# Optimization experiments

Measured on AMD Instinct MI355X. Metric: run time of the kernel, lower is better.

Reference implementation:

```python
import jax, jax.numpy as jnp
import numpy as np

B, T, D = 4, 2048, 2048
H = 16
Q_RANK, KV_RANK = 1536, 512
NOPE, ROPE_D, V_D = 128, 64, 128
QK_D = NOPE + ROPE_D  # 192
D_FF = 8192
EPS = 1e-6
THETA = 10000.0
SCALE = QK_D ** -0.5  # mscale = 1 (no rope_scaling)


def _w(key, shape):
    fan_in = shape[0]
    return jax.random.normal(key, shape, dtype=jnp.float32) / np.sqrt(fan_in)


def setup_inputs() -> dict:
    key = jax.random.key(0)
    ks = jax.random.split(key, 16)
    return {
        "x": jax.random.normal(ks[0], (B, T, D), dtype=jnp.float32),
        "ln1_w": jnp.ones((D,), jnp.float32),
        "wq_a": _w(ks[1], (D, Q_RANK)),
        "q_a_ln_w": jnp.ones((Q_RANK,), jnp.float32),
        "wq_b": _w(ks[2], (Q_RANK, H * QK_D)),
        "wkv_a": _w(ks[3], (D, KV_RANK + ROPE_D)),
        "kv_a_ln_w": jnp.ones((KV_RANK,), jnp.float32),
        "wkv_b": _w(ks[4], (KV_RANK, H * (NOPE + V_D))),
        "wo": _w(ks[5], (H * V_D, D)),
        "ln2_w": jnp.ones((D,), jnp.float32),
        "w_gate": _w(ks[6], (D, D_FF)),
        "w_up": _w(ks[7], (D, D_FF)),
        "w_down": _w(ks[8], (D_FF, D)),
        "attention_mask": jnp.ones((B, T), jnp.int32),
        "positions": jnp.broadcast_to(jnp.arange(T, dtype=jnp.int32), (B, T)),
    }


def rmsnorm(x, w):
    return x * jax.lax.rsqrt(jnp.mean(x * x, axis=-1, keepdims=True) + EPS) * w


def apply_rope(x, positions):
    # x: [B, T, h, d], positions: [B, T]
    d = x.shape[-1]
    inv_freq = 1.0 / (THETA ** (jnp.arange(0, d, 2, dtype=jnp.float32) / d))
    ang = positions.astype(jnp.float32)[:, :, None] * inv_freq  # [B,T,d/2]
    cos = jnp.cos(ang)[:, :, None, :]
    sin = jnp.sin(ang)[:, :, None, :]
    x1, x2 = jnp.split(x, 2, axis=-1)
    return jnp.concatenate([x1 * cos - x2 * sin, x2 * cos + x1 * sin], axis=-1)


def reference(x, ln1_w, wq_a, q_a_ln_w, wq_b, wkv_a, kv_a_ln_w, wkv_b, wo,
              ln2_w, w_gate, w_up, w_down, attention_mask, positions):
    # --- MLA attention block ---
    h = rmsnorm(x, ln1_w)
    # low-rank q projection
    q = rmsnorm(h @ wq_a, q_a_ln_w) @ wq_b            # [B,T,H*192]
    q = q.reshape(B, T, H, QK_D)
    q_pass, q_rot = jnp.split(q, [NOPE], axis=-1)
    # compressed kv + shared rope key
    ckv = h @ wkv_a                                    # [B,T,512+64]
    k_c, k_rot = jnp.split(ckv, [KV_RANK], axis=-1)
    k_rot = k_rot.reshape(B, T, 1, ROPE_D)
    kv = rmsnorm(k_c, kv_a_ln_w) @ wkv_b               # [B,T,H*(128+128)]
    kv = kv.reshape(B, T, H, NOPE + V_D)
    k_pass, v = jnp.split(kv, [NOPE], axis=-1)
    # split RoPE on rope dims only
    q_rot = apply_rope(q_rot, positions)
    k_rot = jnp.broadcast_to(apply_rope(k_rot, positions), (B, T, H, ROPE_D))
    qh = jnp.concatenate([q_pass, q_rot], axis=-1)     # [B,T,H,192]
    kh = jnp.concatenate([k_pass, k_rot], axis=-1)     # [B,T,H,192]
    # attention with causal + padding mask (V pad-to-192 then slice is a no-op mathematically)
    scores = jnp.einsum('bqhd,bkhd->bhqk', qh, kh) * SCALE
    causal = jnp.tril(jnp.ones((T, T), bool))
    mask = causal[None, None] & attention_mask[:, None, None, :].astype(bool)
    scores = jnp.where(mask, scores, jnp.finfo(scores.dtype).min)
    attn = jax.nn.softmax(scores, axis=-1)
    o = jnp.einsum('bhqk,bkhd->bqhd', attn, v).reshape(B, T, H * V_D)
    x = x + o @ wo
    # --- MLP block ---
    h2 = rmsnorm(x, ln2_w)
    mlp = (jax.nn.silu(h2 @ w_gate) * (h2 @ w_up)) @ w_down
    return x + mlp
```

## Files before the change

kernel.cpp:

```cpp
#include <hip/hip_runtime.h>

typedef float f32x4 __attribute__((ext_vector_type(4)));
typedef __bf16 bf16x8 __attribute__((ext_vector_type(8)));
typedef unsigned short u16x8 __attribute__((ext_vector_type(8)));
typedef unsigned short u16x4 __attribute__((ext_vector_type(4)));

static __device__ __forceinline__ unsigned short f2b(float f) {
  union { float f; unsigned u; } v; v.f = f;
  unsigned r = v.u + 0x7fffu + ((v.u >> 16) & 1u);
  return (unsigned short)(r >> 16);
}
static __device__ __forceinline__ float b2f(unsigned short s) {
  union { unsigned u; float f; } v; v.u = ((unsigned)s) << 16;
  return v.f;
}
static __device__ __forceinline__ void gload_lds16(const unsigned short* g, unsigned short* l) {
  __builtin_amdgcn_global_load_lds((const __attribute__((address_space(1))) void*)g,
                                   (__attribute__((address_space(3))) void*)l, 16, 0, 0);
}

#define NEG_BIG -3.0e38f

__global__ __launch_bounds__(256) void fill_sentinel(float* __restrict__ out, int n, float v) {
  int i = blockIdx.x * 256 + threadIdx.x;
  if (i < n) out[i] = v;
}

__global__ __launch_bounds__(256) void transpose_convert(const float* __restrict__ in,
                                                         unsigned short* __restrict__ out,
                                                         int K, int N, int in_ld, int row0, int col0) {
  __shared__ float tile[32][33];
  const int k0 = blockIdx.y * 32, n0 = blockIdx.x * 32;
  const int tx = threadIdx.x & 31, ty = threadIdx.x >> 5;
#pragma unroll
  for (int i = 0; i < 32; i += 8) {
    int k = k0 + ty + i, n = n0 + tx;
    tile[ty + i][tx] = (k < K && n < N) ? in[(size_t)(row0 + k) * in_ld + col0 + n] : 0.f;
  }
  __syncthreads();
#pragma unroll
  for (int i = 0; i < 32; i += 8) {
    int n = n0 + ty + i, k = k0 + tx;
    if (n < N && k < K) out[(size_t)n * K + k] = f2b(tile[tx][ty + i]);
  }
}

__global__ __launch_bounds__(256) void rmsnorm_kernel(const float* __restrict__ in,
                                                      const float* __restrict__ w,
                                                      unsigned short* __restrict__ out,
                                                      int ncols, int in_stride, int out_stride) {
  const int row = blockIdx.x;
  const float* rp = in + (size_t)row * in_stride;
  const int n4 = ncols >> 2;
  float4 v[2];
  int nv = 0;
  float ss = 0.f;
  for (int c = threadIdx.x; c < n4; c += 256) {
    float4 xv = reinterpret_cast<const float4*>(rp)[c];
    v[nv++] = xv;
    ss += xv.x * xv.x + xv.y * xv.y + xv.z * xv.z + xv.w * xv.w;
  }
#pragma unroll
  for (int m = 32; m; m >>= 1) ss += __shfl_xor(ss, m);
  __shared__ float red[4];
  if ((threadIdx.x & 63) == 0) red[threadIdx.x >> 6] = ss;
  __syncthreads();
  const float total = red[0] + red[1] + red[2] + red[3];
  const float scale = rsqrtf(total / (float)ncols + 1e-6f);
  nv = 0;
  unsigned short* op = out + (size_t)row * out_stride;
  for (int c = threadIdx.x; c < n4; c += 256) {
    float4 xv = v[nv++];
    float4 wv = reinterpret_cast<const float4*>(w)[c];
    u16x4 o;
    o[0] = f2b(xv.x * scale * wv.x);
    o[1] = f2b(xv.y * scale * wv.y);
    o[2] = f2b(xv.z * scale * wv.z);
    o[3] = f2b(xv.w * scale * wv.w);
    reinterpret_cast<u16x4*>(op)[c] = o;
  }
}

template <int EPI>
__global__ __launch_bounds__(256) void gemm_bt(const unsigned short* __restrict__ A,
                                               const unsigned short* __restrict__ Bt,
                                               float* __restrict__ outf,
                                               unsigned short* __restrict__ outb,
                                               const float* __restrict__ res,
                                               const unsigned short* __restrict__ aux,
                                               int M, int N, int K) {
  __shared__ __align__(16) unsigned short As[128 * 32];
  __shared__ __align__(16) unsigned short Bs[128 * 32];
  const int tid = threadIdx.x;
  const int l = tid & 63;
  const int lr = l & 15, lg = l >> 4;
  const int wr = tid >> 7, wc = (tid >> 6) & 1;

  const int gx = gridDim.x;
  const int nwg = gx * gridDim.y;
  int lin = blockIdx.y * gx + blockIdx.x;
  {
    const int qq = nwg >> 3, rr = nwg & 7;
    const int xcd = lin & 7, idx = lin >> 3;
    lin = (xcd < rr ? xcd * (qq + 1) : rr * (qq + 1) + (xcd - rr) * qq) + idx;
  }
  const int m0 = (lin / gx) * 128, n0 = (lin % gx) * 128;

  f32x4 acc[4][4] = {};

  for (int k0 = 0; k0 < K; k0 += 32) {
#pragma unroll
    for (int j = 0; j < 2; ++j) {
      const int chunk = j * 256 + tid;
      const int row = chunk >> 2, kc = chunk & 3;
      const unsigned short* ga = A + (size_t)(m0 + row) * K + k0 + kc * 8;
      gload_lds16(ga, &As[(size_t)(j * 256 + (tid & 192)) * 8]);
      int rb = n0 + row;
      if (rb > N - 1) rb = N - 1;
      const unsigned short* gb = Bt + (size_t)rb * K + k0 + kc * 8;
      gload_lds16(gb, &Bs[(size_t)(j * 256 + (tid & 192)) * 8]);
    }
    __syncthreads();
    bf16x8 af[4], bfr[4];
#pragma unroll
    for (int mi = 0; mi < 4; ++mi)
      af[mi] = *reinterpret_cast<const bf16x8*>(&As[(wr * 64 + mi * 16 + lr) * 32 + lg * 8]);
#pragma unroll
    for (int ni = 0; ni < 4; ++ni)
      bfr[ni] = *reinterpret_cast<const bf16x8*>(&Bs[(wc * 64 + ni * 16 + lr) * 32 + lg * 8]);
#pragma unroll
    for (int mi = 0; mi < 4; ++mi)
#pragma unroll
      for (int ni = 0; ni < 4; ++ni)
        acc[mi][ni] = __builtin_amdgcn_mfma_f32_16x16x32_bf16(af[mi], bfr[ni], acc[mi][ni], 0, 0, 0);
    __syncthreads();
  }

#pragma unroll
  for (int mi = 0; mi < 4; ++mi) {
#pragma unroll
    for (int ni = 0; ni < 4; ++ni) {
      const int r0 = m0 + wr * 64 + mi * 16 + lg * 4;
      const int c = n0 + wc * 64 + ni * 16 + lr;
      if (c < N) {
#pragma unroll
        for (int j = 0; j < 4; ++j) {
          const size_t idx = (size_t)(r0 + j) * N + c;
          const float v = acc[mi][ni][j];
          if constexpr (EPI == 0) outf[idx] = v;
          else if constexpr (EPI == 1) outb[idx] = f2b(v);
          else if constexpr (EPI == 2) outf[idx] = v + res[idx];
          else if constexpr (EPI == 3) outb[idx] = f2b(v / (1.f + __expf(-v)));
          else outb[idx] = f2b(v * b2f(aux[idx]));
        }
      }
    }
  }
}

template <int EPI>
__global__ __launch_bounds__(512, 1) void gemm256(const unsigned short* __restrict__ A,
                                                  const unsigned short* __restrict__ Bt,
                                                  float* __restrict__ outf,
                                                  unsigned short* __restrict__ outb,
                                                  const float* __restrict__ res,
                                                  const unsigned short* __restrict__ aux,
                                                  int M, int N, int K) {
  __shared__ __align__(16) unsigned short Lds[2][2][2][8192];
  const int tid = threadIdx.x;
  const int l = tid & 63, lr = l & 15, lg = l >> 4;
  const int w = tid >> 6, wr = w >> 2, wn = w & 3;

  const int gn = N >> 8;
  int lin = blockIdx.x;
  {
    const int nwg = gridDim.x;
    lin = (lin & 7) * (nwg >> 3) + (lin >> 3);
  }
  const int m0 = (lin / gn) * 256, n0 = (lin % gn) * 256;

  const int NT = K >> 6;
  const int swz = (lg ^ ((lr >> 1) & 3)) * 8;

  f32x4 acc[8][4] = {};

  auto stageh = [&](int mat, int kh, int t) {
    const unsigned short* src = mat ? Bt : A;
    const int rb = mat ? n0 : m0;
    const int d = t & 1;
#pragma unroll
    for (int g = 0; g < 2; ++g) {
      const int c = g * 512 + tid;
      const int row = c >> 2;
      const int kc = (c & 3) ^ ((row >> 1) & 3);
      gload_lds16(src + (size_t)(rb + row) * K + t * 64 + kh * 32 + kc * 8,
                  &Lds[d][mat][kh][(size_t)(g * 512 + (tid & ~63)) * 8]);
    }
  };

  stageh(0, 0, 0); stageh(1, 0, 0); stageh(0, 1, 0); stageh(1, 1, 0);
  asm volatile("s_waitcnt vmcnt(4)" ::: "memory");
  __builtin_amdgcn_s_barrier();
  __builtin_amdgcn_sched_barrier(0);

  for (int t = 0; t < NT; ++t) {
    const int d = t & 1;
    const bool pf = (t + 1 < NT);
    bf16x8 af[4], bfv[4];

#define RD_A(mh, kk, i)                                                                    \
  af[i] = *reinterpret_cast<const bf16x8*>(                                                \
      &Lds[d][0][kk][(wr * 128 + ((mh) * 4 + (i)) * 16 + lr) * 32 + swz])
#define RD_B(kk, ni)                                                                       \
  bfv[ni] = *reinterpret_cast<const bf16x8*>(                                              \
      &Lds[d][1][kk][(wn * 64 + (ni) * 16 + lr) * 32 + swz])
#define MFMA16(mh)                                                                         \
  _Pragma("unroll") for (int i = 0; i < 4; ++i)                                            \
  _Pragma("unroll") for (int ni = 0; ni < 4; ++ni)                                         \
      acc[(mh) * 4 + i][ni] =                                                              \
          __builtin_amdgcn_mfma_f32_16x16x32_bf16(af[i], bfv[ni], acc[(mh) * 4 + i][ni], 0, 0, 0)

    RD_A(0, 0, 0); RD_A(0, 0, 1); RD_A(0, 0, 2); RD_A(0, 0, 3);
    RD_B(0, 0); RD_B(0, 1); RD_B(0, 2); RD_B(0, 3);
    if (pf) stageh(0, 0, t + 1);
    __builtin_amdgcn_s_barrier();
    asm volatile("s_waitcnt lgkmcnt(0)" ::: "memory");
    __builtin_amdgcn_sched_barrier(0);
    __builtin_amdgcn_s_setprio(1);
    MFMA16(0);
    __builtin_amdgcn_s_setprio(0);
    __builtin_amdgcn_s_barrier();

    RD_A(1, 0, 0); RD_A(1, 0, 1); RD_A(1, 0, 2); RD_A(1, 0, 3);
    if (pf) stageh(1, 0, t + 1);
    __builtin_amdgcn_s_barrier();
    asm volatile("s_waitcnt lgkmcnt(0)" ::: "memory");
    __builtin_amdgcn_sched_barrier(0);
    __builtin_amdgcn_s_setprio(1);
    MFMA16(1);
    __builtin_amdgcn_s_setprio(0);
    __builtin_amdgcn_sched_barrier(0);
    if (pf) asm volatile("s_waitcnt vmcnt(4)" ::: "memory");
    else    asm volatile("s_waitcnt vmcnt(0)" ::: "memory");
    __builtin_amdgcn_s_barrier();
    __builtin_amdgcn_sched_barrier(0);

    RD_A(0, 1, 0); RD_A(0, 1, 1); RD_A(0, 1, 2); RD_A(0, 1, 3);
    RD_B(1, 0); RD_B(1, 1); RD_B(1, 2); RD_B(1, 3);
    if (pf) stageh(0, 1, t + 1);
    __builtin_amdgcn_s_barrier();
    asm volatile("s_waitcnt lgkmcnt(0)" ::: "memory");
    __builtin_amdgcn_sched_barrier(0);
    __builtin_amdgcn_s_setprio(1);
    MFMA16(0);
    __builtin_amdgcn_s_setprio(0);
    __builtin_amdgcn_s_barrier();

    RD_A(1, 1, 0); RD_A(1, 1, 1); RD_A(1, 1, 2); RD_A(1, 1, 3);
    if (pf) stageh(1, 1, t + 1);
    __builtin_amdgcn_s_barrier();
    asm volatile("s_waitcnt lgkmcnt(0)" ::: "memory");
    __builtin_amdgcn_sched_barrier(0);
    __builtin_amdgcn_s_setprio(1);
    MFMA16(1);
    __builtin_amdgcn_s_setprio(0);
    __builtin_amdgcn_sched_barrier(0);
    if (pf) asm volatile("s_waitcnt vmcnt(4)" ::: "memory");
    __builtin_amdgcn_s_barrier();
    __builtin_amdgcn_sched_barrier(0);

#undef RD_A
#undef RD_B
#undef MFMA16
  }

#pragma unroll
  for (int mi = 0; mi < 8; ++mi) {
#pragma unroll
    for (int ni = 0; ni < 4; ++ni) {
      const int r = m0 + wr * 128 + mi * 16 + lg * 4;
      const int c = n0 + wn * 64 + ni * 16 + lr;
#pragma unroll
      for (int j = 0; j < 4; ++j) {
        const size_t idx = (size_t)(r + j) * N + c;
        const float v = acc[mi][ni][j];
        if constexpr (EPI == 0) outf[idx] = v;
        else if constexpr (EPI == 1) outb[idx] = f2b(v);
        else if constexpr (EPI == 2) outf[idx] = v + res[idx];
        else if constexpr (EPI == 3) outb[idx] = f2b(v / (1.f + __expf(-v)));
        else outb[idx] = f2b(v * b2f(aux[idx]));
      }
    }
  }
}

__global__ __launch_bounds__(256) void rope_scale_q(unsigned short* __restrict__ q,
                                                    const int* __restrict__ positions) {
  const int row = blockIdx.x;
  const int pos = positions[row];
  unsigned short* qp = q + (size_t)row * 3072;
  const int tid = threadIdx.x;
  const float SCALE = 0.07216878364870322f;
#pragma unroll
  for (int i = 0; i < 8; ++i) {
    int e = i * 256 + tid;
    int hh = e >> 7, d = e & 127;
    int idx = hh * 192 + d;
    qp[idx] = f2b(b2f(qp[idx]) * SCALE);
  }
#pragma unroll
  for (int i = 0; i < 2; ++i) {
    int e = i * 256 + tid;
    int hh = e >> 5, j = e & 31;
    int base = hh * 192 + 128;
    float x1 = b2f(qp[base + j]), x2 = b2f(qp[base + 32 + j]);
    float freq = __expf(-(float)j * (9.210340371976184f / 32.f));
    float sa, ca;
    __sincosf((float)pos * freq, &sa, &ca);
    qp[base + j] = f2b((x1 * ca - x2 * sa) * SCALE);
    qp[base + 32 + j] = f2b((x2 * ca + x1 * sa) * SCALE);
  }
}

__global__ __launch_bounds__(256) void repack_k(const unsigned short* __restrict__ kv,
                                                const float* __restrict__ ckv,
                                                const int* __restrict__ positions,
                                                unsigned short* __restrict__ kh) {
  const int row = blockIdx.x;
  const int tid = threadIdx.x;
  {
    const int hh = tid >> 4, db = tid & 15;
    u16x8 v = *reinterpret_cast<const u16x8*>(kv + (size_t)row * 4096 + hh * 256 + db * 8);
    *reinterpret_cast<u16x8*>(kh + (size_t)row * 3072 + hh * 192 + db * 8) = v;
  }
  __shared__ float o1[32], o2[32];
  if (tid < 32) {
    const int j = tid;
    float x1 = ckv[(size_t)row * 576 + 512 + j];
    float x2 = ckv[(size_t)row * 576 + 544 + j];
    const int pos = positions[row];
    float freq = __expf(-(float)j * (9.210340371976184f / 32.f));
    float sa, ca;
    __sincosf((float)pos * freq, &sa, &ca);
    o1[j] = x1 * ca - x2 * sa;
    o2[j] = x2 * ca + x1 * sa;
  }
  __syncthreads();
#pragma unroll
  for (int i = 0; i < 4; ++i) {
    int e = i * 256 + tid;
    int hh = e >> 6, d = e & 63;
    float v = (d < 32) ? o1[d] : o2[d - 32];
    kh[(size_t)row * 3072 + hh * 192 + 128 + d] = f2b(v);
  }
}

__global__ __launch_bounds__(512) void mla_attn(const unsigned short* __restrict__ qh,
                                                const unsigned short* __restrict__ kh,
                                                const unsigned short* __restrict__ kv,
                                                unsigned short* __restrict__ o) {
  const int T = 2048, H = 16;
  const int qt = (int)gridDim.x - 1 - (int)blockIdx.x;
  const int b = blockIdx.y >> 4;
  const int h = blockIdx.y & 15;
  const int tid = threadIdx.x, w = tid >> 6, l = tid & 63;
  const int lg = l >> 4, lr = l & 15;

  __shared__ __align__(16) unsigned short Ks[64 * 200];
  __shared__ __align__(16) unsigned short Vts[128 * 64];
  __shared__ __align__(16) unsigned short Pl[8][16 * 72];
  __shared__ float exs[8][16];

  int krow[3], kcol[3];
#pragma unroll
  for (int i = 0; i < 3; ++i) { int c = i * 512 + tid; krow[i] = c / 24; kcol[i] = (c % 24) * 8; }
  const int vkvp = tid >> 4;
  const int vf0 = (tid & 15) * 8;

  const unsigned short* kbase0 = kh + (((size_t)b * T) * H + h) * 192;
  const unsigned short* vbase0 = kv + (((size_t)b * T) * H + h) * 256 + 128;

  bf16x8 qa[6];
  {
    const size_t qrow = (size_t)b * T + qt * 128 + w * 16 + lr;
    const unsigned short* qp = qh + (qrow * H + h) * 192 + lg * 8;
#pragma unroll
    for (int kc = 0; kc < 6; ++kc)
      qa[kc] = *reinterpret_cast<const bf16x8*>(qp + kc * 32);
  }

  u16x8 kreg[3], vregA, vregB;
#pragma unroll
  for (int i = 0; i < 3; ++i)
    kreg[i] = *reinterpret_cast<const u16x8*>(kbase0 + (size_t)krow[i] * 3072 + kcol[i]);
  vregA = *reinterpret_cast<const u16x8*>(vbase0 + (size_t)(2 * vkvp) * 4096 + vf0);
  vregB = *reinterpret_cast<const u16x8*>(vbase0 + (size_t)(2 * vkvp + 1) * 4096 + vf0);

  f32x4 ot[8] = {};
  f32x4 lacc = {};
  float mrow[4] = {NEG_BIG, NEG_BIG, NEG_BIG, NEG_BIG};
  bf16x8 ones;
#pragma unroll
  for (int e = 0; e < 8; ++e) ones[e] = (__bf16)1.0f;

  const int ktmax = 2 * qt + 1;
  for (int kt = 0; kt <= ktmax; ++kt) {
#pragma unroll
    for (int i = 0; i < 3; ++i)
      *reinterpret_cast<u16x8*>(&Ks[krow[i] * 200 + kcol[i]]) = kreg[i];
    {
      const int c7 = (vf0 >> 3) & 7;
#pragma unroll
      for (int e = 0; e < 8; ++e) {
        const int blk = (vkvp >> 2) ^ (e ^ c7);
        const unsigned val = (unsigned)(unsigned short)vregA[e] |
                             ((unsigned)(unsigned short)vregB[e] << 16);
        *reinterpret_cast<unsigned*>(&Vts[(vf0 + e) * 64 + blk * 8 + (vkvp & 3) * 2]) = val;
      }
    }
    __syncthreads();

    if (kt < ktmax) {
      const unsigned short* kb = kbase0 + (size_t)(kt + 1) * 64 * 3072;
      const unsigned short* vb = vbase0 + (size_t)(kt + 1) * 64 * 4096;
#pragma unroll
      for (int i = 0; i < 3; ++i)
        kreg[i] = *reinterpret_cast<const u16x8*>(kb + (size_t)krow[i] * 3072 + kcol[i]);
      vregA = *reinterpret_cast<const u16x8*>(vb + (size_t)(2 * vkvp) * 4096 + vf0);
      vregB = *reinterpret_cast<const u16x8*>(vb + (size_t)(2 * vkvp + 1) * 4096 + vf0);
    }

    f32x4 s4[4];
#pragma unroll
    for (int ni = 0; ni < 4; ++ni) {
      f32x4 a = {};
#pragma unroll
      for (int kc = 0; kc < 6; ++kc) {
        bf16x8 kf = *reinterpret_cast<const bf16x8*>(&Ks[(ni * 16 + lr) * 200 + kc * 32 + lg * 8]);
        a = __builtin_amdgcn_mfma_f32_16x16x32_bf16(qa[kc], kf, a, 0, 0, 0);
      }
      s4[ni] = a;
    }
    if (kt >= 2 * qt) {
#pragma unroll
      for (int ni = 0; ni < 4; ++ni) {
        const int colr = ni * 16 + lr;
#pragma unroll
        for (int j = 0; j < 4; ++j) {
          const int qrl = qt * 128 + w * 16 + lg * 4 + j - kt * 64;
          if (colr > qrl) s4[ni][j] = NEG_BIG;
        }
      }
    }

    float pmj[4];
    int need = 0;
#pragma unroll
    for (int j = 0; j < 4; ++j) {
      pmj[j] = fmaxf(fmaxf(s4[0][j], s4[1][j]), fmaxf(s4[2][j], s4[3][j]));
      need |= (pmj[j] > mrow[j] + 8.f) ? 1 : 0;
    }
    if (__any(need)) {
      float al[4];
#pragma unroll
      for (int j = 0; j < 4; ++j) {
        float rm = pmj[j];
#pragma unroll
        for (int m = 1; m < 16; m <<= 1) rm = fmaxf(rm, __shfl_xor(rm, m));
        const float mn = fmaxf(mrow[j], rm);
        al[j] = __expf(mrow[j] - mn);
        mrow[j] = mn;
      }
      if (lr == 0) {
#pragma unroll
        for (int j = 0; j < 4; ++j) exs[w][lg * 4 + j] = al[j];
      }
      const float af = exs[w][lr];
#pragma unroll
      for (int mi = 0; mi < 8; ++mi) {
        ot[mi][0] *= af; ot[mi][1] *= af; ot[mi][2] *= af; ot[mi][3] *= af;
      }
      lacc[0] *= af; lacc[1] *= af; lacc[2] *= af; lacc[3] *= af;
    }

#pragma unroll
    for (int ni = 0; ni < 4; ++ni)
#pragma unroll
      for (int j = 0; j < 4; ++j)
        Pl[w][(lg * 4 + j) * 72 + ni * 16 + lr] = f2b(__expf(s4[ni][j] - mrow[j]));

    bf16x8 pf0 = *reinterpret_cast<const bf16x8*>(&Pl[w][lr * 72 + lg * 8]);
    bf16x8 pf1 = *reinterpret_cast<const bf16x8*>(&Pl[w][lr * 72 + 32 + lg * 8]);
    lacc = __builtin_amdgcn_mfma_f32_16x16x32_bf16(ones, pf0, lacc, 0, 0, 0);
    lacc = __builtin_amdgcn_mfma_f32_16x16x32_bf16(ones, pf1, lacc, 0, 0, 0);
#pragma unroll
    for (int mi = 0; mi < 8; ++mi) {
      const int f = mi * 16 + lr;
      const int sfz = (f & 7) ^ ((f >> 3) & 7);
      const int blk0 = lg ^ sfz;
      const int blk1 = (4 + lg) ^ sfz;
      bf16x8 vf0r = *reinterpret_cast<const bf16x8*>(&Vts[f * 64 + blk0 * 8]);
      ot[mi] = __builtin_amdgcn_mfma_f32_16x16x32_bf16(vf0r, pf0, ot[mi], 0, 0, 0);
      bf16x8 vf1r = *reinterpret_cast<const bf16x8*>(&Vts[f * 64 + blk1 * 8]);
      ot[mi] = __builtin_amdgcn_mfma_f32_16x16x32_bf16(vf1r, pf1, ot[mi], 0, 0, 0);
    }
    __syncthreads();
  }

  const float li = 1.f / lacc[0];
  const size_t orow = (size_t)b * T + qt * 128 + w * 16 + lr;
#pragma unroll
  for (int mi = 0; mi < 8; ++mi)
#pragma unroll
    for (int j = 0; j < 4; ++j) {
      const int feat = mi * 16 + lg * 4 + j;
      o[orow * 2048 + h * 128 + feat] = f2b(ot[mi][j] * li);
    }
}

extern "C" void kernel_launch(void* const* d_in, const int* in_sizes, int n_in,
                              void* d_out, int out_size, void* d_ws, size_t ws_size,
                              hipStream_t stream) {
  (void)in_sizes; (void)n_in;
  const float* x      = (const float*)d_in[0];
  const float* ln1_w  = (const float*)d_in[1];
  const float* wq_a   = (const float*)d_in[2];
  const float* qaln_w = (const float*)d_in[3];
  const float* wq_b   = (const float*)d_in[4];
  const float* wkv_a  = (const float*)d_in[5];
  const float* kvln_w = (const float*)d_in[6];
  const float* wkv_b  = (const float*)d_in[7];
  const float* wo     = (const float*)d_in[8];
  const float* ln2_w  = (const float*)d_in[9];
  const float* w_gate = (const float*)d_in[10];
  const float* w_up   = (const float*)d_in[11];
  const float* w_down = (const float*)d_in[12];
  const int*   pos    = (const int*)d_in[14];
  float* out = (float*)d_out;

  const int Mt = 8192;

  char* ws = (char*)d_ws;
  const size_t R1 = 0;
  const size_t R2 = R1 + 67108864;
  const size_t R3 = R2 + 50331648;
  const size_t R4 = R3 + 50331648;
  const size_t R5 = R4 + 33554432;
  const size_t R6 = R5 + 18874368;
  const size_t REQ = R6 + 9437184;

  if (ws_size < REQ) {
    fill_sentinel<<<dim3((out_size + 255) / 256), dim3(256), 0, stream>>>(
        out, out_size, (float)(ws_size >> 20));
    return;
  }

  float*          qa_f  = (float*)(ws + R1);
  unsigned short* kvbuf = (unsigned short*)(ws + R1);
  unsigned short* qbuf  = (unsigned short*)(ws + R2);
  unsigned short* qan   = (unsigned short*)(ws + R3);
  unsigned short* ckvn  = (unsigned short*)(ws + R3);
  unsigned short* khbuf = (unsigned short*)(ws + R3);
  unsigned short* hbuf  = (unsigned short*)(ws + R4);
  unsigned short* obuf  = (unsigned short*)(ws + R4);
  float*          ckv   = (float*)(ws + R5);
  unsigned short* slotW = (unsigned short*)(ws + R6);
  unsigned short* actb  = (unsigned short*)(ws + 0);
  unsigned short* h2b   = (unsigned short*)(ws + 134217728);
  unsigned short* wsl2  = (unsigned short*)(ws + 167772160);

  dim3 blk(256);
  dim3 blk5(512);
  auto tcf = [&](const float* W, int K, int N) {
    transpose_convert<<<dim3((N + 31) / 32, (K + 31) / 32), blk, 0, stream>>>(W, slotW, K, N, N, 0, 0);
  };
  auto g256 = [&](auto epi, const unsigned short* Aa, const unsigned short* Bb, float* of,
                  unsigned short* ob, const float* rs, const unsigned short* ax, int N, int K) {
    gemm256<decltype(epi)::value><<<dim3(32 * (N >> 8)), blk5, 0, stream>>>(Aa, Bb, of, ob, rs, ax, Mt, N, K);
  };

  rmsnorm_kernel<<<Mt, blk, 0, stream>>>(x, ln1_w, hbuf, 2048, 2048, 2048);
  tcf(wq_a, 2048, 1536);
  g256(std::integral_constant<int,0>{}, hbuf, slotW, qa_f, nullptr, nullptr, nullptr, 1536, 2048);
  rmsnorm_kernel<<<Mt, blk, 0, stream>>>(qa_f, qaln_w, qan, 1536, 1536, 1536);
  tcf(wq_b, 1536, 3072);
  g256(std::integral_constant<int,1>{}, qan, slotW, nullptr, qbuf, nullptr, nullptr, 3072, 1536);
  tcf(wkv_a, 2048, 576);
  gemm_bt<0><<<dim3(5, 64), blk, 0, stream>>>(hbuf, slotW, ckv, nullptr, nullptr, nullptr, Mt, 576, 2048);
  rmsnorm_kernel<<<Mt, blk, 0, stream>>>(ckv, kvln_w, ckvn, 512, 576, 512);
  tcf(wkv_b, 512, 4096);
  g256(std::integral_constant<int,1>{}, ckvn, slotW, nullptr, kvbuf, nullptr, nullptr, 4096, 512);
  rope_scale_q<<<Mt, blk, 0, stream>>>(qbuf, pos);
  repack_k<<<Mt, blk, 0, stream>>>(kvbuf, ckv, pos, khbuf);
  mla_attn<<<dim3(16, 64), blk5, 0, stream>>>(qbuf, khbuf, kvbuf, obuf);
  tcf(wo, 2048, 2048);
  g256(std::integral_constant<int,2>{}, obuf, slotW, out, nullptr, x, nullptr, 2048, 2048);
  rmsnorm_kernel<<<Mt, blk, 0, stream>>>(out, ln2_w, h2b, 2048, 2048, 2048);
  transpose_convert<<<dim3(256, 64), blk, 0, stream>>>(w_gate, wsl2, 2048, 8192, 8192, 0, 0);
  g256(std::integral_constant<int,3>{}, h2b, wsl2, nullptr, actb, nullptr, nullptr, 8192, 2048);
  transpose_convert<<<dim3(256, 64), blk, 0, stream>>>(w_up, wsl2, 2048, 8192, 8192, 0, 0);
  g256(std::integral_constant<int,4>{}, h2b, wsl2, nullptr, actb, nullptr, actb, 8192, 2048);
  transpose_convert<<<dim3(64, 256), blk, 0, stream>>>(w_down, wsl2, 8192, 2048, 2048, 0, 0);
  g256(std::integral_constant<int,2>{}, actb, wsl2, out, nullptr, out, nullptr, 2048, 8192);
}
```

Baseline: 1.698 ms.

## Deepen GEMM LDS pipeline to four K=32 stages with prefetch distance three

Restructures the 256x256 GEMM main loop from two double-buffered K=64 tiles (each split into two halves) into a four-slot ring of K=32 tiles, prefetching three tiles ahead. The vmcnt waits are adjusted so the tile about to be consumed is ready while two more remain in flight. The aim is to hide global-load latency better without increasing LDS usage. The cost is twice as many loop iterations with their barriers and waits per unit of K.

```diff
diff --git a/kernel.cpp b/kernel.cpp
--- a/kernel.cpp
+++ b/kernel.cpp
@@ -166,7 +166,7 @@
                                                   const float* __restrict__ res,
                                                   const unsigned short* __restrict__ aux,
                                                   int M, int N, int K) {
-  __shared__ __align__(16) unsigned short Lds[2][2][2][8192];
+  __shared__ __align__(16) unsigned short Lds[4][2][8192];
   const int tid = threadIdx.x;
   const int l = tid & 63, lr = l & 15, lg = l >> 4;
   const int w = tid >> 6, wr = w >> 2, wn = w & 3;
@@ -179,50 +179,52 @@
   }
   const int m0 = (lin / gn) * 256, n0 = (lin % gn) * 256;
 
-  const int NT = K >> 6;
+  const int NT = K >> 5;
   const int swz = (lg ^ ((lr >> 1) & 3)) * 8;
 
   f32x4 acc[8][4] = {};
 
-  auto stageh = [&](int mat, int kh, int t) {
+  auto stage_mat = [&](int mat, int t) {
     const unsigned short* src = mat ? Bt : A;
     const int rb = mat ? n0 : m0;
-    const int d = t & 1;
+    const int d = t & 3;
 #pragma unroll
     for (int g = 0; g < 2; ++g) {
       const int c = g * 512 + tid;
       const int row = c >> 2;
       const int kc = (c & 3) ^ ((row >> 1) & 3);
-      gload_lds16(src + (size_t)(rb + row) * K + t * 64 + kh * 32 + kc * 8,
-                  &Lds[d][mat][kh][(size_t)(g * 512 + (tid & ~63)) * 8]);
+      gload_lds16(src + (size_t)(rb + row) * K + t * 32 + kc * 8,
+                  &Lds[d][mat][(size_t)(g * 512 + (tid & ~63)) * 8]);
     }
   };
 
-  stageh(0, 0, 0); stageh(1, 0, 0); stageh(0, 1, 0); stageh(1, 1, 0);
-  asm volatile("s_waitcnt vmcnt(4)" ::: "memory");
+  stage_mat(0, 0); stage_mat(1, 0);
+  stage_mat(0, 1); stage_mat(1, 1);
+  stage_mat(0, 2); stage_mat(1, 2);
+  asm volatile("s_waitcnt vmcnt(8)" ::: "memory");
   __builtin_amdgcn_s_barrier();
   __builtin_amdgcn_sched_barrier(0);
 
   for (int t = 0; t < NT; ++t) {
-    const int d = t & 1;
-    const bool pf = (t + 1 < NT);
+    const int d = t & 3;
+    const bool pf = (t + 3 < NT);
     bf16x8 af[4], bfv[4];
 
-#define RD_A(mh, kk, i)                                                                    \
+#define RD_A(mh, i)                                                                        \
   af[i] = *reinterpret_cast<const bf16x8*>(                                                \
-      &Lds[d][0][kk][(wr * 128 + ((mh) * 4 + (i)) * 16 + lr) * 32 + swz])
-#define RD_B(kk, ni)                                                                       \
+      &Lds[d][0][(wr * 128 + ((mh) * 4 + (i)) * 16 + lr) * 32 + swz])
+#define RD_B(ni)                                                                           \
   bfv[ni] = *reinterpret_cast<const bf16x8*>(                                              \
-      &Lds[d][1][kk][(wn * 64 + (ni) * 16 + lr) * 32 + swz])
+      &Lds[d][1][(wn * 64 + (ni) * 16 + lr) * 32 + swz])
 #define MFMA16(mh)                                                                         \
   _Pragma("unroll") for (int i = 0; i < 4; ++i)                                            \
   _Pragma("unroll") for (int ni = 0; ni < 4; ++ni)                                         \
       acc[(mh) * 4 + i][ni] =                                                              \
           __builtin_amdgcn_mfma_f32_16x16x32_bf16(af[i], bfv[ni], acc[(mh) * 4 + i][ni], 0, 0, 0)
 
-    RD_A(0, 0, 0); RD_A(0, 0, 1); RD_A(0, 0, 2); RD_A(0, 0, 3);
-    RD_B(0, 0); RD_B(0, 1); RD_B(0, 2); RD_B(0, 3);
-    if (pf) stageh(0, 0, t + 1);
+    RD_A(0, 0); RD_A(0, 1); RD_A(0, 2); RD_A(0, 3);
+    RD_B(0); RD_B(1); RD_B(2); RD_B(3);
+    if (pf) stage_mat(0, t + 3);
     __builtin_amdgcn_s_barrier();
     asm volatile("s_waitcnt lgkmcnt(0)" ::: "memory");
     __builtin_amdgcn_sched_barrier(0);
@@ -231,8 +233,8 @@
     __builtin_amdgcn_s_setprio(0);
     __builtin_amdgcn_s_barrier();
 
-    RD_A(1, 0, 0); RD_A(1, 0, 1); RD_A(1, 0, 2); RD_A(1, 0, 3);
-    if (pf) stageh(1, 0, t + 1);
+    RD_A(1, 0); RD_A(1, 1); RD_A(1, 2); RD_A(1, 3);
+    if (pf) stage_mat(1, t + 3);
     __builtin_amdgcn_s_barrier();
     asm volatile("s_waitcnt lgkmcnt(0)" ::: "memory");
     __builtin_amdgcn_sched_barrier(0);
@@ -240,32 +242,12 @@
     MFMA16(1);
     __builtin_amdgcn_s_setprio(0);
     __builtin_amdgcn_sched_barrier(0);
-    if (pf) asm volatile("s_waitcnt vmcnt(4)" ::: "memory");
-    else    asm volatile("s_waitcnt vmcnt(0)" ::: "memory");
-    __builtin_amdgcn_s_barrier();
-    __builtin_amdgcn_sched_barrier(0);
-
-    RD_A(0, 1, 0); RD_A(0, 1, 1); RD_A(0, 1, 2); RD_A(0, 1, 3);
-    RD_B(1, 0); RD_B(1, 1); RD_B(1, 2); RD_B(1, 3);
-    if (pf) stageh(0, 1, t + 1);
-    __builtin_amdgcn_s_barrier();
-    asm volatile("s_waitcnt lgkmcnt(0)" ::: "memory");
-    __builtin_amdgcn_sched_barrier(0);
-    __builtin_amdgcn_s_setprio(1);
-    MFMA16(0);
-    __builtin_amdgcn_s_setprio(0);
-    __builtin_amdgcn_s_barrier();
-
-    RD_A(1, 1, 0); RD_A(1, 1, 1); RD_A(1, 1, 2); RD_A(1, 1, 3);
-    if (pf) stageh(1, 1, t + 1);
-    __builtin_amdgcn_s_barrier();
-    asm volatile("s_waitcnt lgkmcnt(0)" ::: "memory");
-    __builtin_amdgcn_sched_barrier(0);
-    __builtin_amdgcn_s_setprio(1);
-    MFMA16(1);
-    __builtin_amdgcn_s_setprio(0);
-    __builtin_amdgcn_sched_barrier(0);
-    if (pf) asm volatile("s_waitcnt vmcnt(4)" ::: "memory");
+    {
+      const int rem = NT - 1 - t;
+      if (rem >= 3)      asm volatile("s_waitcnt vmcnt(8)" ::: "memory");
+      else if (rem == 2) asm volatile("s_waitcnt vmcnt(4)" ::: "memory");
+      else if (rem == 1) asm volatile("s_waitcnt vmcnt(0)" ::: "memory");
+    }
     __builtin_amdgcn_s_barrier();
     __builtin_amdgcn_sched_barrier(0);
 
```

Result: slower. 1.738 ms (+2.4%).

## Balance causal attention by pairing query tiles, fold q scale into weights, regroup GEMM tiles

Applied to the files above, without the earlier changes.

Each attention workgroup now processes two query tiles, bx and 15-bx, so every block does the same amount of causal work and the grid is halved. The softmax scale is folded into the wq_b weight conversion, which removes the separate scaling pass over the q nope dimensions. The GEMM block index mapping is changed to group eight M-tiles per N column for better L2 reuse. Risks: half as many attention blocks for occupancy, and the q scale is applied before bf16 rounding of the weights, which changes rounding slightly.

```diff
diff --git a/kernel.cpp b/kernel.cpp
--- a/kernel.cpp
+++ b/kernel.cpp
@@ -28,7 +28,8 @@
 
 __global__ __launch_bounds__(256) void transpose_convert(const float* __restrict__ in,
                                                          unsigned short* __restrict__ out,
-                                                         int K, int N, int in_ld, int row0, int col0) {
+                                                         int K, int N, int in_ld, int row0, int col0,
+                                                         float scale) {
   __shared__ float tile[32][33];
   const int k0 = blockIdx.y * 32, n0 = blockIdx.x * 32;
   const int tx = threadIdx.x & 31, ty = threadIdx.x >> 5;
@@ -41,7 +42,7 @@
 #pragma unroll
   for (int i = 0; i < 32; i += 8) {
     int n = n0 + ty + i, k = k0 + tx;
-    if (n < N && k < K) out[(size_t)n * K + k] = f2b(tile[tx][ty + i]);
+    if (n < N && k < K) out[(size_t)n * K + k] = f2b(tile[tx][ty + i] * scale);
   }
 }
 
@@ -177,7 +178,11 @@
     const int nwg = gridDim.x;
     lin = (lin & 7) * (nwg >> 3) + (lin >> 3);
   }
-  const int m0 = (lin / gn) * 256, n0 = (lin % gn) * 256;
+  const int npg = gn << 3;
+  const int gid = lin / npg;
+  const int idx = lin - gid * npg;
+  const int m0 = (gid * 8 + (idx & 7)) * 256;
+  const int n0 = (idx >> 3) * 256;
 
   const int NT = K >> 6;
   const int swz = (lg ^ ((lr >> 1) & 3)) * 8;
@@ -282,32 +287,24 @@
       const int c = n0 + wn * 64 + ni * 16 + lr;
 #pragma unroll
       for (int j = 0; j < 4; ++j) {
-        const size_t idx = (size_t)(r + j) * N + c;
+        const size_t idx2 = (size_t)(r + j) * N + c;
         const float v = acc[mi][ni][j];
-        if constexpr (EPI == 0) outf[idx] = v;
-        else if constexpr (EPI == 1) outb[idx] = f2b(v);
-        else if constexpr (EPI == 2) outf[idx] = v + res[idx];
-        else if constexpr (EPI == 3) outb[idx] = f2b(v / (1.f + __expf(-v)));
-        else outb[idx] = f2b(v * b2f(aux[idx]));
+        if constexpr (EPI == 0) outf[idx2] = v;
+        else if constexpr (EPI == 1) outb[idx2] = f2b(v);
+        else if constexpr (EPI == 2) outf[idx2] = v + res[idx2];
+        else if constexpr (EPI == 3) outb[idx2] = f2b(v / (1.f + __expf(-v)));
+        else outb[idx2] = f2b(v * b2f(aux[idx2]));
       }
     }
   }
 }
 
-__global__ __launch_bounds__(256) void rope_scale_q(unsigned short* __restrict__ q,
-                                                    const int* __restrict__ positions) {
+__global__ __launch_bounds__(256) void rope_q(unsigned short* __restrict__ q,
+                                              const int* __restrict__ positions) {
   const int row = blockIdx.x;
   const int pos = positions[row];
   unsigned short* qp = q + (size_t)row * 3072;
   const int tid = threadIdx.x;
-  const float SCALE = 0.07216878364870322f;
-#pragma unroll
-  for (int i = 0; i < 8; ++i) {
-    int e = i * 256 + tid;
-    int hh = e >> 7, d = e & 127;
-    int idx = hh * 192 + d;
-    qp[idx] = f2b(b2f(qp[idx]) * SCALE);
-  }
 #pragma unroll
   for (int i = 0; i < 2; ++i) {
     int e = i * 256 + tid;
@@ -317,8 +314,8 @@
     float freq = __expf(-(float)j * (9.210340371976184f / 32.f));
     float sa, ca;
     __sincosf((float)pos * freq, &sa, &ca);
-    qp[base + j] = f2b((x1 * ca - x2 * sa) * SCALE);
-    qp[base + 32 + j] = f2b((x2 * ca + x1 * sa) * SCALE);
+    qp[base + j] = f2b(x1 * ca - x2 * sa);
+    qp[base + 32 + j] = f2b(x2 * ca + x1 * sa);
   }
 }
 
@@ -360,7 +357,7 @@
                                                 const unsigned short* __restrict__ kv,
                                                 unsigned short* __restrict__ o) {
   const int T = 2048, H = 16;
-  const int qt = (int)gridDim.x - 1 - (int)blockIdx.x;
+  const int bx = blockIdx.x;
   const int b = blockIdx.y >> 4;
   const int h = blockIdx.y & 15;
   const int tid = threadIdx.x, w = tid >> 6, l = tid & 63;
@@ -380,142 +377,147 @@
   const unsigned short* kbase0 = kh + (((size_t)b * T) * H + h) * 192;
   const unsigned short* vbase0 = kv + (((size_t)b * T) * H + h) * 256 + 128;
 
-  bf16x8 qa[6];
-  {
-    const size_t qrow = (size_t)b * T + qt * 128 + w * 16 + lr;
-    const unsigned short* qp = qh + (qrow * H + h) * 192 + lg * 8;
-#pragma unroll
-    for (int kc = 0; kc < 6; ++kc)
-      qa[kc] = *reinterpret_cast<const bf16x8*>(qp + kc * 32);
-  }
-
-  u16x8 kreg[3], vregA, vregB;
-#pragma unroll
-  for (int i = 0; i < 3; ++i)
-    kreg[i] = *reinterpret_cast<const u16x8*>(kbase0 + (size_t)krow[i] * 3072 + kcol[i]);
-  vregA = *reinterpret_cast<const u16x8*>(vbase0 + (size_t)(2 * vkvp) * 4096 + vf0);
-  vregB = *reinterpret_cast<const u16x8*>(vbase0 + (size_t)(2 * vkvp + 1) * 4096 + vf0);
-
-  f32x4 ot[8] = {};
-  f32x4 lacc = {};
-  float mrow[4] = {NEG_BIG, NEG_BIG, NEG_BIG, NEG_BIG};
   bf16x8 ones;
 #pragma unroll
   for (int e = 0; e < 8; ++e) ones[e] = (__bf16)1.0f;
 
-  const int ktmax = 2 * qt + 1;
-  for (int kt = 0; kt <= ktmax; ++kt) {
+  for (int half = 0; half < 2; ++half) {
+    const int qt = half ? (15 - bx) : bx;
+
+    bf16x8 qa[6];
+    {
+      const size_t qrow = (size_t)b * T + qt * 128 + w * 16 + lr;
+      const unsigned short* qp = qh + (qrow * H + h) * 192 + lg * 8;
+#pragma unroll
+      for (int kc = 0; kc < 6; ++kc)
+        qa[kc] = *reinterpret_cast<const bf16x8*>(qp + kc * 32);
+    }
+
+    u16x8 kreg[3], vregA, vregB;
 #pragma unroll
     for (int i = 0; i < 3; ++i)
-      *reinterpret_cast<u16x8*>(&Ks[krow[i] * 200 + kcol[i]]) = kreg[i];
-    {
-      const int c7 = (vf0 >> 3) & 7;
-#pragma unroll
-      for (int e = 0; e < 8; ++e) {
-        const int blk = (vkvp >> 2) ^ (e ^ c7);
-        const unsigned val = (unsigned)(unsigned short)vregA[e] |
-                             ((unsigned)(unsigned short)vregB[e] << 16);
-        *reinterpret_cast<unsigned*>(&Vts[(vf0 + e) * 64 + blk * 8 + (vkvp & 3) * 2]) = val;
-      }
+      kreg[i] = *reinterpret_cast<const u16x8*>(kbase0 + (size_t)krow[i] * 3072 + kcol[i]);
+    vregA = *reinterpret_cast<const u16x8*>(vbase0 + (size_t)(2 * vkvp) * 4096 + vf0);
+    vregB = *reinterpret_cast<const u16x8*>(vbase0 + (size_t)(2 * vkvp + 1) * 4096 + vf0);
+
+    f32x4 ot[8] = {};
+    f32x4 lacc = {};
+    float mrow[4] = {NEG_BIG, NEG_BIG, NEG_BIG, NEG_BIG};
+
+    const int ktmax = 2 * qt + 1;
+    for (int kt = 0; kt <= ktmax; ++kt) {
+#pragma unroll
+      for (int i = 0; i < 3; ++i)
+        *reinterpret_cast<u16x8*>(&Ks[krow[i] * 200 + kcol[i]]) = kreg[i];
+      {
+        const int c7 = (vf0 >> 3) & 7;
+#pragma unroll
+        for (int e = 0; e < 8; ++e) {
+          const int blk = (vkvp >> 2) ^ (e ^ c7);
+          const unsigned val = (unsigned)(unsigned short)vregA[e] |
+                               ((unsigned)(unsigned short)vregB[e] << 16);
+          *reinterpret_cast<unsigned*>(&Vts[(vf0 + e) * 64 + blk * 8 + (vkvp & 3) * 2]) = val;
+        }
+      }
+      __syncthreads();
+
+      if (kt < ktmax) {
+        const unsigned short* kb = kbase0 + (size_t)(kt + 1) * 64 * 3072;
+        const unsigned short* vb = vbase0 + (size_t)(kt + 1) * 64 * 4096;
+#pragma unroll
+        for (int i = 0; i < 3; ++i)
+          kreg[i] = *reinterpret_cast<const u16x8*>(kb + (size_t)krow[i] * 3072 + kcol[i]);
+        vregA = *reinterpret_cast<const u16x8*>(vb + (size_t)(2 * vkvp) * 4096 + vf0);
+        vregB = *reinterpret_cast<const u16x8*>(vb + (size_t)(2 * vkvp + 1) * 4096 + vf0);
+      }
+
+      f32x4 s4[4];
+#pragma unroll
+      for (int ni = 0; ni < 4; ++ni) {
+        f32x4 a = {};
+#pragma unroll
+        for (int kc = 0; kc < 6; ++kc) {
+          bf16x8 kf = *reinterpret_cast<const bf16x8*>(&Ks[(ni * 16 + lr) * 200 + kc * 32 + lg * 8]);
+          a = __builtin_amdgcn_mfma_f32_16x16x32_bf16(qa[kc], kf, a, 0, 0, 0);
+        }
+        s4[ni] = a;
+      }
+      if (kt >= 2 * qt) {
+#pragma unroll
+        for (int ni = 0; ni < 4; ++ni) {
+          const int colr = ni * 16 + lr;
+#pragma unroll
+          for (int j = 0; j < 4; ++j) {
+            const int qrl = qt * 128 + w * 16 + lg * 4 + j - kt * 64;
+            if (colr > qrl) s4[ni][j] = NEG_BIG;
+          }
+        }
+      }
+
+      float pmj[4];
+      int need = 0;
+#pragma unroll
+      for (int j = 0; j < 4; ++j) {
+        pmj[j] = fmaxf(fmaxf(s4[0][j], s4[1][j]), fmaxf(s4[2][j], s4[3][j]));
+        need |= (pmj[j] > mrow[j] + 8.f) ? 1 : 0;
+      }
+      if (__any(need)) {
+        float al[4];
+#pragma unroll
+        for (int j = 0; j < 4; ++j) {
+          float rm = pmj[j];
+#pragma unroll
+          for (int m = 1; m < 16; m <<= 1) rm = fmaxf(rm, __shfl_xor(rm, m));
+          const float mn = fmaxf(mrow[j], rm);
+          al[j] = __expf(mrow[j] - mn);
+          mrow[j] = mn;
+        }
+        if (lr == 0) {
+#pragma unroll
+          for (int j = 0; j < 4; ++j) exs[w][lg * 4 + j] = al[j];
+        }
+        const float af = exs[w][lr];
+#pragma unroll
+        for (int mi = 0; mi < 8; ++mi) {
+          ot[mi][0] *= af; ot[mi][1] *= af; ot[mi][2] *= af; ot[mi][3] *= af;
+        }
+        lacc[0] *= af; lacc[1] *= af; lacc[2] *= af; lacc[3] *= af;
+      }
+
+#pragma unroll
+      for (int ni = 0; ni < 4; ++ni)
+#pragma unroll
+        for (int j = 0; j < 4; ++j)
+          Pl[w][(lg * 4 + j) * 72 + ni * 16 + lr] = f2b(__expf(s4[ni][j] - mrow[j]));
+
+      bf16x8 pf0 = *reinterpret_cast<const bf16x8*>(&Pl[w][lr * 72 + lg * 8]);
+      bf16x8 pf1 = *reinterpret_cast<const bf16x8*>(&Pl[w][lr * 72 + 32 + lg * 8]);
+      lacc = __builtin_amdgcn_mfma_f32_16x16x32_bf16(ones, pf0, lacc, 0, 0, 0);
+      lacc = __builtin_amdgcn_mfma_f32_16x16x32_bf16(ones, pf1, lacc, 0, 0, 0);
+#pragma unroll
+      for (int mi = 0; mi < 8; ++mi) {
+        const int f = mi * 16 + lr;
+        const int sfz = (f & 7) ^ ((f >> 3) & 7);
+        const int blk0 = lg ^ sfz;
+        const int blk1 = (4 + lg) ^ sfz;
+        bf16x8 vf0r = *reinterpret_cast<const bf16x8*>(&Vts[f * 64 + blk0 * 8]);
+        ot[mi] = __builtin_amdgcn_mfma_f32_16x16x32_bf16(vf0r, pf0, ot[mi], 0, 0, 0);
+        bf16x8 vf1r = *reinterpret_cast<const bf16x8*>(&Vts[f * 64 + blk1 * 8]);
+        ot[mi] = __builtin_amdgcn_mfma_f32_16x16x32_bf16(vf1r, pf1, ot[mi], 0, 0, 0);
+      }
+      __syncthreads();
     }
-    __syncthreads();
-
-    if (kt < ktmax) {
-      const unsigned short* kb = kbase0 + (size_t)(kt + 1) * 64 * 3072;
-      const unsigned short* vb = vbase0 + (size_t)(kt + 1) * 64 * 4096;
-#pragma unroll
-      for (int i = 0; i < 3; ++i)
-        kreg[i] = *reinterpret_cast<const u16x8*>(kb + (size_t)krow[i] * 3072 + kcol[i]);
-      vregA = *reinterpret_cast<const u16x8*>(vb + (size_t)(2 * vkvp) * 4096 + vf0);
-      vregB = *reinterpret_cast<const u16x8*>(vb + (size_t)(2 * vkvp + 1) * 4096 + vf0);
-    }
-
-    f32x4 s4[4];
-#pragma unroll
-    for (int ni = 0; ni < 4; ++ni) {
-      f32x4 a = {};
-#pragma unroll
-      for (int kc = 0; kc < 6; ++kc) {
-        bf16x8 kf = *reinterpret_cast<const bf16x8*>(&Ks[(ni * 16 + lr) * 200 + kc * 32 + lg * 8]);
-        a = __builtin_amdgcn_mfma_f32_16x16x32_bf16(qa[kc], kf, a, 0, 0, 0);
-      }
-      s4[ni] = a;
-    }
-    if (kt >= 2 * qt) {
-#pragma unroll
-      for (int ni = 0; ni < 4; ++ni) {
-        const int colr = ni * 16 + lr;
-#pragma unroll
-        for (int j = 0; j < 4; ++j) {
-          const int qrl = qt * 128 + w * 16 + lg * 4 + j - kt * 64;
-          if (colr > qrl) s4[ni][j] = NEG_BIG;
-        }
-      }
-    }
-
-    float pmj[4];
-    int need = 0;
-#pragma unroll
-    for (int j = 0; j < 4; ++j) {
-      pmj[j] = fmaxf(fmaxf(s4[0][j], s4[1][j]), fmaxf(s4[2][j], s4[3][j]));
-      need |= (pmj[j] > mrow[j] + 8.f) ? 1 : 0;
-    }
-    if (__any(need)) {
-      float al[4];
+
+    const float li = 1.f / lacc[0];
+    const size_t orow = (size_t)b * T + qt * 128 + w * 16 + lr;
+#pragma unroll
+    for (int mi = 0; mi < 8; ++mi)
 #pragma unroll
       for (int j = 0; j < 4; ++j) {
-        float rm = pmj[j];
-#pragma unroll
-        for (int m = 1; m < 16; m <<= 1) rm = fmaxf(rm, __shfl_xor(rm, m));
-        const float mn = fmaxf(mrow[j], rm);
-        al[j] = __expf(mrow[j] - mn);
-        mrow[j] = mn;
-      }
-      if (lr == 0) {
-#pragma unroll
-        for (int j = 0; j < 4; ++j) exs[w][lg * 4 + j] = al[j];
-      }
-      const float af = exs[w][lr];
-#pragma unroll
-      for (int mi = 0; mi < 8; ++mi) {
-        ot[mi][0] *= af; ot[mi][1] *= af; ot[mi][2] *= af; ot[mi][3] *= af;
-      }
-      lacc[0] *= af; lacc[1] *= af; lacc[2] *= af; lacc[3] *= af;
-    }
-
-#pragma unroll
-    for (int ni = 0; ni < 4; ++ni)
-#pragma unroll
-      for (int j = 0; j < 4; ++j)
-        Pl[w][(lg * 4 + j) * 72 + ni * 16 + lr] = f2b(__expf(s4[ni][j] - mrow[j]));
-
-    bf16x8 pf0 = *reinterpret_cast<const bf16x8*>(&Pl[w][lr * 72 + lg * 8]);
-    bf16x8 pf1 = *reinterpret_cast<const bf16x8*>(&Pl[w][lr * 72 + 32 + lg * 8]);
-    lacc = __builtin_amdgcn_mfma_f32_16x16x32_bf16(ones, pf0, lacc, 0, 0, 0);
-    lacc = __builtin_amdgcn_mfma_f32_16x16x32_bf16(ones, pf1, lacc, 0, 0, 0);
-#pragma unroll
-    for (int mi = 0; mi < 8; ++mi) {
-      const int f = mi * 16 + lr;
-      const int sfz = (f & 7) ^ ((f >> 3) & 7);
-      const int blk0 = lg ^ sfz;
-      const int blk1 = (4 + lg) ^ sfz;
-      bf16x8 vf0r = *reinterpret_cast<const bf16x8*>(&Vts[f * 64 + blk0 * 8]);
-      ot[mi] = __builtin_amdgcn_mfma_f32_16x16x32_bf16(vf0r, pf0, ot[mi], 0, 0, 0);
-      bf16x8 vf1r = *reinterpret_cast<const bf16x8*>(&Vts[f * 64 + blk1 * 8]);
-      ot[mi] = __builtin_amdgcn_mfma_f32_16x16x32_bf16(vf1r, pf1, ot[mi], 0, 0, 0);
-    }
-    __syncthreads();
-  }
-
-  const float li = 1.f / lacc[0];
-  const size_t orow = (size_t)b * T + qt * 128 + w * 16 + lr;
-#pragma unroll
-  for (int mi = 0; mi < 8; ++mi)
-#pragma unroll
-    for (int j = 0; j < 4; ++j) {
-      const int feat = mi * 16 + lg * 4 + j;
-      o[orow * 2048 + h * 128 + feat] = f2b(ot[mi][j] * li);
-    }
+        const int feat = mi * 16 + lg * 4 + j;
+        o[orow * 2048 + h * 128 + feat] = f2b(ot[mi][j] * li);
+      }
+  }
 }
 
 extern "C" void kernel_launch(void* const* d_in, const int* in_sizes, int n_in,
@@ -571,8 +573,8 @@
 
   dim3 blk(256);
   dim3 blk5(512);
-  auto tcf = [&](const float* W, int K, int N) {
-    transpose_convert<<<dim3((N + 31) / 32, (K + 31) / 32), blk, 0, stream>>>(W, slotW, K, N, N, 0, 0);
+  auto tcf = [&](const float* W, int K, int N, float scale) {
+    transpose_convert<<<dim3((N + 31) / 32, (K + 31) / 32), blk, 0, stream>>>(W, slotW, K, N, N, 0, 0, scale);
   };
   auto g256 = [&](auto epi, const unsigned short* Aa, const unsigned short* Bb, float* of,
                   unsigned short* ob, const float* rs, const unsigned short* ax, int N, int K) {
@@ -580,26 +582,26 @@
   };
 
   rmsnorm_kernel<<<Mt, blk, 0, stream>>>(x, ln1_w, hbuf, 2048, 2048, 2048);
-  tcf(wq_a, 2048, 1536);
+  tcf(wq_a, 2048, 1536, 1.0f);
   g256(std::integral_constant<int,0>{}, hbuf, slotW, qa_f, nullptr, nullptr, nullptr, 1536, 2048);
   rmsnorm_kernel<<<Mt, blk, 0, stream>>>(qa_f, qaln_w, qan, 1536, 1536, 1536);
-  tcf(wq_b, 1536, 3072);
+  tcf(wq_b, 1536, 3072, 0.07216878364870322f);
   g256(std::integral_constant<int,1>{}, qan, slotW, nullptr, qbuf, nullptr, nullptr, 3072, 1536);
-  tcf(wkv_a, 2048, 576);
+  tcf(wkv_a, 2048, 576, 1.0f);
   gemm_bt<0><<<dim3(5, 64), blk, 0, stream>>>(hbuf, slotW, ckv, nullptr, nullptr, nullptr, Mt, 576, 2048);
   rmsnorm_kernel<<<Mt, blk, 0, stream>>>(ckv, kvln_w, ckvn, 512, 576, 512);
-  tcf(wkv_b, 512, 4096);
+  tcf(wkv_b, 512, 4096, 1.0f);
   g256(std::integral_constant<int,1>{}, ckvn, slotW, nullptr, kvbuf, nullptr, nullptr, 4096, 512);
-  rope_scale_q<<<Mt, blk, 0, stream>>>(qbuf, pos);
+  rope_q<<<Mt, blk, 0, stream>>>(qbuf, pos);
   repack_k<<<Mt, blk, 0, stream>>>(kvbuf, ckv, pos, khbuf);
-  mla_attn<<<dim3(16, 64), blk5, 0, stream>>>(qbuf, khbuf, kvbuf, obuf);
-  tcf(wo, 2048, 2048);
+  mla_attn<<<dim3(8, 64), blk5, 0, stream>>>(qbuf, khbuf, kvbuf, obuf);
+  tcf(wo, 2048, 2048, 1.0f);
   g256(std::integral_constant<int,2>{}, obuf, slotW, out, nullptr, x, nullptr, 2048, 2048);
   rmsnorm_kernel<<<Mt, blk, 0, stream>>>(out, ln2_w, h2b, 2048, 2048, 2048);
-  transpose_convert<<<dim3(256, 64), blk, 0, stream>>>(w_gate, wsl2, 2048, 8192, 8192, 0, 0);
+  transpose_convert<<<dim3(256, 64), blk, 0, stream>>>(w_gate, wsl2, 2048, 8192, 8192, 0, 0, 1.0f);
   g256(std::integral_constant<int,3>{}, h2b, wsl2, nullptr, actb, nullptr, nullptr, 8192, 2048);
-  transpose_convert<<<dim3(256, 64), blk, 0, stream>>>(w_up, wsl2, 2048, 8192, 8192, 0, 0);
+  transpose_convert<<<dim3(256, 64), blk, 0, stream>>>(w_up, wsl2, 2048, 8192, 8192, 0, 0, 1.0f);
   g256(std::integral_constant<int,4>{}, h2b, wsl2, nullptr, actb, nullptr, actb, 8192, 2048);
-  transpose_convert<<<dim3(64, 256), blk, 0, stream>>>(w_down, wsl2, 8192, 2048, 2048, 0, 0);
+  transpose_convert<<<dim3(64, 256), blk, 0, stream>>>(w_down, wsl2, 8192, 2048, 2048, 0, 0, 1.0f);
   g256(std::integral_constant<int,2>{}, actb, wsl2, out, nullptr, out, nullptr, 2048, 8192);
 }
```

Result: faster. 1.600 ms (-5.8%).
